# Kernel optimization log

Hardware: AMD Instinct MI355X
Metric: run time of the kernel (lower is better)

## Reference

```python
import jax, jax.numpy as jnp
import numpy as np

B, L, H, W = 4, 5000, 256, 256
C_IN, DIM_LOI, N_PTS0, N_PTS1, DIM_FC, N_OUT_LINE = 256, 128, 32, 8, 1024, 2500
SCALE = N_PTS0 // N_PTS1  # MaxPool1d kernel/stride


def setup_inputs() -> dict:
    key = jax.random.key(0)
    ks = jax.random.split(key, 8)
    feature = jax.random.normal(ks[0], (B, C_IN, H, W), jnp.float32)
    # line endpoints in pixel coords of the 256x256 feature map
    lines = jax.random.uniform(ks[1], (B, L, 2, 2), jnp.float32) * (H - 1)
    s = lambda fan: 1.0 / np.sqrt(fan)
    fc1_w = (jax.random.normal(ks[2], (DIM_LOI, C_IN), jnp.float32) * s(C_IN))
    fc1_b = jnp.zeros((DIM_LOI,), jnp.float32)
    w1 = jax.random.normal(ks[3], (DIM_LOI * N_PTS1, DIM_FC), jnp.float32) * s(DIM_LOI * N_PTS1)
    b1 = jnp.zeros((DIM_FC,), jnp.float32)
    w2 = jax.random.normal(ks[4], (DIM_FC, DIM_FC), jnp.float32) * s(DIM_FC)
    b2 = jnp.zeros((DIM_FC,), jnp.float32)
    w3 = jax.random.normal(ks[5], (DIM_FC, 4), jnp.float32) * s(DIM_FC)
    b3 = jnp.zeros((4,), jnp.float32)
    return dict(feature=feature, lines=lines, fc1_w=fc1_w, fc1_b=fc1_b,
                w1=w1, b1=b1, w2=w2, b2=b2, w3=w3, b3=b3)


def reference(feature, lines, fc1_w, fc1_b, w1, b1, w2, b2, w3, b3):
    # fc1: 1x1 conv  [B,C_IN,H,W] -> [B,DIM_LOI,H,W]
    x = jnp.einsum('bchw,oc->bohw', feature, fc1_w) + fc1_b[None, :, None, None]

    # sample N_PTS0 points along each line (lerp between endpoints), minus 0.5
    lam = jnp.linspace(0.0, 1.0, N_PTS0, dtype=feature.dtype)[None, None, :, None]
    p = lines[:, :, 0:1, :] * lam + lines[:, :, 1:2, :] * (1.0 - lam) - 0.5  # [B,L,P,2]
    px, py = p[..., 0], p[..., 1]  # px indexes H (rows), py indexes W (cols)
    px0 = jnp.clip(jnp.floor(px), 0.0, H - 1.0)
    py0 = jnp.clip(jnp.floor(py), 0.0, W - 1.0)
    px1 = jnp.clip(px0 + 1.0, 0.0, H - 1.0)
    py1 = jnp.clip(py0 + 1.0, 0.0, W - 1.0)
    ix0, iy0 = px0.astype(jnp.int32), py0.astype(jnp.int32)
    ix1, iy1 = px1.astype(jnp.int32), py1.astype(jnp.int32)
    idx00 = ix0 * W + iy0
    idx10 = ix1 * W + iy0
    idx01 = ix0 * W + iy1
    idx11 = ix1 * W + iy1
    w00 = (px1 - px) * (py1 - py)
    w10 = (px - px0) * (py1 - py)
    w01 = (px1 - px) * (py - py0)
    w11 = (px - px0) * (py - py0)

    def gather_one(fmap, i00, i10, i01, i11, g00, g10, g01, g11):
        f = fmap.reshape(DIM_LOI, H * W)
        g = lambda idx: f[:, idx.reshape(-1)].reshape(DIM_LOI, L, N_PTS0)
        return g(i00) * g00 + g(i10) * g10 + g(i01) * g01 + g(i11) * g11

    xp = jax.vmap(gather_one)(x, idx00, idx10, idx01, idx11, w00, w10, w01, w11)
    # xp: [B, DIM_LOI, L, N_PTS0] -> maxpool along points -> [B, DIM_LOI, L, N_PTS1]
    xp = xp.reshape(B, DIM_LOI, L, N_PTS1, SCALE).max(-1)
    # reshape like torch: [N, DIM_LOI, N_PTS1] -> [N, DIM_LOI*N_PTS1] (channel-major)
    feat = xp.transpose(0, 2, 1, 3).reshape(B, L, DIM_LOI * N_PTS1)

    # fc2 MLP -> 4 logits
    h = jax.nn.relu(feat @ w1 + b1)
    h = jax.nn.relu(h @ w2 + b2)
    logits = h @ w3 + b3  # [B, L, 4]
    s = jax.nn.softmax(logits, axis=-1)

    # threshold conditions
    keep = ((s[..., 1] > 0.25) | (s[..., 2] > 0.25) | (s[..., 3] > 0.25)) & (s[..., 0] < 0.25)

    def select(p0, s0, m):
        cnt = m.sum()
        key = jnp.where(m, jnp.argmax(s0, -1), -1)  # masked-out get -1 -> sorted last
        order = jnp.argsort(-key)  # stable desc sort of argmax class
        idx = order[jnp.arange(N_OUT_LINE) % jnp.maximum(cnt, 1)]
        lo = jnp.where(cnt > 0, p0[idx], 0.0)
        so = jnp.where(cnt > 0, s0[idx], 0.0)
        return lo, so

    lines_out, score_out = jax.vmap(select)(lines, s, keep)
    return lines_out, score_out, s
```

## Files before the change

### kernel.cpp

```cpp
#include <hip/hip_runtime.h>
#include <cstdint>
#include <cstddef>

#define B_     4
#define L_     5000
#define H_     256
#define W_     256
#define HW_    65536
#define CIN_   256
#define DLOI_  128
#define NPTS0_ 32
#define NPTS1_ 8
#define DFC_   1024
#define NOUT_  2500
#define M_     (B_*L_)
#define MPAD_  20096
#define NBAND_ 157

typedef _Float16 f16;
typedef _Float16 f16x4 __attribute__((ext_vector_type(4)));
typedef _Float16 f16x8 __attribute__((ext_vector_type(8)));
typedef float    f32x4 __attribute__((ext_vector_type(4)));

__device__ __forceinline__ void gload16(const void* g, void* l) {
  __builtin_amdgcn_global_load_lds(
      (const __attribute__((address_space(1))) void*)g,
      (__attribute__((address_space(3))) void*)l, 16, 0, 0);
}

__global__ __launch_bounds__(256) void k_wsplit(const float* __restrict__ src,
                                                f16* __restrict__ h,
                                                f16* __restrict__ l) {
  int i = (blockIdx.x * 256 + threadIdx.x) * 4;
  float4 v = *(const float4*)(src + i);
  f16 h0 = (f16)v.x, h1 = (f16)v.y, h2 = (f16)v.z, h3 = (f16)v.w;
  *(f16x4*)(h + i) = (f16x4){h0, h1, h2, h3};
  *(f16x4*)(l + i) = (f16x4){(f16)(v.x - (float)h0), (f16)(v.y - (float)h1),
                             (f16)(v.z - (float)h2), (f16)(v.w - (float)h3)};
}

__global__ __launch_bounds__(1024) void k_order(const float* __restrict__ lines,
                                                int* __restrict__ perm) {
  __shared__ int hist[64];
  __shared__ int off[64];
  const int b = blockIdx.x;
  const int t = threadIdx.x;
  if (t < 64) hist[t] = 0;
  __syncthreads();
  int mycell[5];
  #pragma unroll
  for (int i = 0; i < 5; i++) {
    const int l = t * 5 + i;
    int cell = -1;
    if (l < L_) {
      const float* ln = lines + (size_t)(b * L_ + l) * 4;
      float mx = 0.5f * (ln[0] + ln[2]);
      float my = 0.5f * (ln[1] + ln[3]);
      int cx = min(max((int)mx, 0), 255) >> 5;
      int cy = min(max((int)my, 0), 255) >> 5;
      cell = (cx & 1) | ((cy & 1) << 1) | ((cx & 2) << 1) | ((cy & 2) << 2)
           | ((cx & 4) << 2) | ((cy & 4) << 3);
      atomicAdd(&hist[cell], 1);
    }
    mycell[i] = cell;
  }
  __syncthreads();
  if (t == 0) {
    int s = 0;
    for (int c = 0; c < 64; c++) { off[c] = s; s += hist[c]; }
  }
  __syncthreads();
  #pragma unroll
  for (int i = 0; i < 5; i++) {
    if (mycell[i] >= 0) {
      int slot = atomicAdd(&off[mycell[i]], 1);
      perm[b * L_ + slot] = t * 5 + i;
    }
  }
}

__global__ __launch_bounds__(256) void k_conv_mfma(const float* __restrict__ fin,
                                                   const f16* __restrict__ wh,
                                                   const f16* __restrict__ wl,
                                                   const float* __restrict__ bias,
                                                   float* __restrict__ xout) {
  __shared__ f16 lds[16384];
  const int t = threadIdx.x;
  const int P0 = blockIdx.x * 128;
  const int b  = P0 >> 16;
  const int ph0 = P0 & 65535;
  const int lane = t & 63, wave = t >> 6;
  const int quad = lane >> 4, lo = lane & 15;
  const int wm = wave >> 1, wn = wave & 1;

  const int c_base = (t & 7) * 4;
  const int p = (t >> 3) * 4;
  const size_t fbase = (size_t)b * CIN_ * HW_ + (size_t)ph0 + p;

  const int srow = t >> 2;
  const int skb  = (t & 3) * 16;
  const char* gBh = (const char*)wh + (size_t)srow * 512 + skb;
  const char* gBl = (const char*)wl + (size_t)srow * 512 + skb;
  char* ldsB = (char*)lds + t * 16;

  f32x4 acc[4][4];
  #pragma unroll
  for (int mt = 0; mt < 4; mt++)
    #pragma unroll
    for (int nt = 0; nt < 4; nt++) acc[mt][nt] = (f32x4){0.f, 0.f, 0.f, 0.f};

  float4 av[4], nv[4];
  #pragma unroll
  for (int j = 0; j < 4; j++)
    av[j] = *(const float4*)(fin + fbase + (size_t)(c_base + j) * HW_);

  for (int kc = 0; kc < 8; kc++) {
    const size_t bko = (size_t)kc * 64;
    gload16(gBh + bko,         ldsB + 16384);
    gload16(gBh + 32768 + bko, ldsB + 16384 + 4096);
    gload16(gBl + bko,         ldsB + 24576);
    gload16(gBl + 32768 + bko, ldsB + 24576 + 4096);

    #pragma unroll
    for (int i = 0; i < 4; i++) {
      f16 hh[4], ll[4];
      #pragma unroll
      for (int j = 0; j < 4; j++) {
        float v = ((const float*)&av[j])[i];
        hh[j] = (f16)v;
        ll[j] = (f16)(v - (float)hh[j]);
      }
      *(f16x4*)(&lds[(p + i) * 32 + c_base])        = (f16x4){hh[0], hh[1], hh[2], hh[3]};
      *(f16x4*)(&lds[4096 + (p + i) * 32 + c_base]) = (f16x4){ll[0], ll[1], ll[2], ll[3]};
    }
    __syncthreads();

    if (kc < 7) {
      #pragma unroll
      for (int j = 0; j < 4; j++)
        nv[j] = *(const float4*)(fin + fbase + (size_t)((kc + 1) * 32 + c_base + j) * HW_);
    }

    f16x8 ah[4], al[4], bh4[4], bl4[4];
    #pragma unroll
    for (int mt = 0; mt < 4; mt++) {
      int row = wm * 64 + mt * 16 + lo;
      ah[mt] = *(const f16x8*)(&lds[row * 32 + quad * 8]);
      al[mt] = *(const f16x8*)(&lds[4096 + row * 32 + quad * 8]);
    }
    #pragma unroll
    for (int nt = 0; nt < 4; nt++) {
      int row = wn * 64 + nt * 16 + lo;
      bh4[nt] = *(const f16x8*)(&lds[8192 + row * 32 + quad * 8]);
      bl4[nt] = *(const f16x8*)(&lds[12288 + row * 32 + quad * 8]);
    }
    #pragma unroll
    for (int mt = 0; mt < 4; mt++)
      #pragma unroll
      for (int nt = 0; nt < 4; nt++) {
        acc[mt][nt] = __builtin_amdgcn_mfma_f32_16x16x32_f16(ah[mt], bh4[nt], acc[mt][nt], 0, 0, 0);
        acc[mt][nt] = __builtin_amdgcn_mfma_f32_16x16x32_f16(ah[mt], bl4[nt], acc[mt][nt], 0, 0, 0);
        acc[mt][nt] = __builtin_amdgcn_mfma_f32_16x16x32_f16(al[mt], bh4[nt], acc[mt][nt], 0, 0, 0);
      }
    __syncthreads();
    #pragma unroll
    for (int j = 0; j < 4; j++) av[j] = nv[j];
  }

  #pragma unroll
  for (int nt = 0; nt < 4; nt++) {
    int col = wn * 64 + nt * 16 + lo;
    float bv = bias[col];
    #pragma unroll
    for (int mt = 0; mt < 4; mt++) {
      int rowb = P0 + wm * 64 + mt * 16 + quad * 4;
      #pragma unroll
      for (int r = 0; r < 4; r++)
        xout[(size_t)(rowb + r) * DLOI_ + col] = acc[mt][nt][r] + bv;
    }
  }
}

__global__ __launch_bounds__(128) void k_sample(const float* __restrict__ x,
                                                const float* __restrict__ lines,
                                                const int* __restrict__ perm,
                                                f16* __restrict__ fh,
                                                f16* __restrict__ fl) {
  __shared__ int4   s_off[NPTS0_];
  __shared__ float4 s_wt [NPTS0_];
  const int blk0 = blockIdx.x;
  const int s = (blk0 & 7) * (M_ / 8) + (blk0 >> 3);
  const int b = s / L_;
  const int row = b * L_ + perm[s];
  const int c = threadIdx.x;
  const float* ln = lines + (size_t)row * 4;

  if (c < NPTS0_) {
    const float e0x = ln[0], e0y = ln[1], e1x = ln[2], e1y = ln[3];
    const int i = c;
    float lam = (float)i * (1.0f / 31.0f);
    float px = e0x * lam + e1x * (1.f - lam) - 0.5f;
    float py = e0y * lam + e1y * (1.f - lam) - 0.5f;
    float px0 = fminf(fmaxf(floorf(px), 0.f), 255.f);
    float py0 = fminf(fmaxf(floorf(py), 0.f), 255.f);
    float px1 = fminf(px0 + 1.f, 255.f);
    float py1 = fminf(py0 + 1.f, 255.f);
    int ix0 = (int)px0, iy0 = (int)py0, ix1 = (int)px1, iy1 = (int)py1;
    s_wt[i]  = make_float4((px1 - px) * (py1 - py),
                           (px - px0) * (py1 - py),
                           (px1 - px) * (py - py0),
                           (px - px0) * (py - py0));
    s_off[i] = make_int4((ix0 * W_ + iy0) * (DLOI_ * 4),
                         (ix1 * W_ + iy0) * (DLOI_ * 4),
                         (ix0 * W_ + iy1) * (DLOI_ * 4),
                         (ix1 * W_ + iy1) * (DLOI_ * 4));
  }
  __syncthreads();

  const char* xbc = (const char*)(x + (size_t)b * HW_ * DLOI_) + c * 4;
  f16x8 vh, vl;
  for (int q = 0; q < NPTS1_; q++) {
    float m = -1e30f;
    #pragma unroll
    for (int r = 0; r < 4; r++) {
      const int i = q * 4 + r;
      const int4   o = s_off[i];
      const float4 w = s_wt[i];
      float v = w.x * *(const float*)(xbc + o.x)
              + w.y * *(const float*)(xbc + o.y)
              + w.z * *(const float*)(xbc + o.z)
              + w.w * *(const float*)(xbc + o.w);
      m = fmaxf(m, v);
    }
    f16 h = (f16)m;
    vh[q] = h;
    vl[q] = (f16)(m - (float)h);
  }
  *(f16x8*)(fh + (size_t)row * DFC_ + c * 8) = vh;
  *(f16x8*)(fl + (size_t)row * DFC_ + c * 8) = vl;
}

__global__ __launch_bounds__(256) void k_tsplit(const float* __restrict__ Wsrc,
                                                f16* __restrict__ Th,
                                                f16* __restrict__ Tl) {
  __shared__ float tile[32][33];
  const int bj = blockIdx.x, bi = blockIdx.y;
  const int tx = threadIdx.x & 31, ty = threadIdx.x >> 5;
  #pragma unroll
  for (int r = ty; r < 32; r += 8)
    tile[r][tx] = Wsrc[(size_t)(bi * 32 + r) * 1024 + bj * 32 + tx];
  __syncthreads();
  #pragma unroll
  for (int r = ty; r < 32; r += 8) {
    float v = tile[tx][r];
    f16 h = (f16)v;
    size_t o = (size_t)(bj * 32 + r) * 1024 + bi * 32 + tx;
    Th[o] = h;
    Tl[o] = (f16)(v - (float)h);
  }
}

#define BKT_    32
#define NTT_    (DFC_/BKT_)
#define SLOT_B_ 32768
#define AH_O_   0
#define AL_O_   8192
#define BH_O_   16384
#define BL_O_   24576

template <bool SPLIT_OUT>
__global__ __launch_bounds__(256, 2) void k_gemm_f16x3(
    const f16* __restrict__ Ah, const f16* __restrict__ Al,
    const f16* __restrict__ Bh, const f16* __restrict__ Bl,
    const float* __restrict__ bias,
    f16* __restrict__ Oh, f16* __restrict__ Ol,
    const float* __restrict__ w3, float* __restrict__ part) {
  __shared__ f16 lds[2 * SLOT_B_ / 2];
  char* ldsc = (char*)lds;

  const int orig = blockIdx.x;
  const int wg = (orig & 7) * 157 + (orig >> 3);
  const int band = wg >> 3;
  const int nb   = wg & 7;
  const int r0 = band * 128;
  const int n0 = nb * 128;

  const int t = threadIdx.x;
  const int lane = t & 63, wave = t >> 6;
  const int quad = lane >> 4, lo = lane & 15;
  const int wm = wave >> 1, wn = wave & 1;

  const uint32_t u0 = (uint32_t)t;
  const uint32_t u1 = (uint32_t)t + 256u;
  const uint32_t us0 = u0 ^ ((u0 >> 3) & 7);
  const uint32_t us1 = u1 ^ ((u1 >> 3) & 7);
  const size_t s0 = (size_t)(us0 >> 2) * 2048 + (size_t)(us0 & 3) * 16;
  const size_t s1 = (size_t)(us1 >> 2) * 2048 + (size_t)(us1 & 3) * 16;

  const char* gAh = (const char*)Ah + (size_t)r0 * 2048;
  const char* gAl = (const char*)Al + (size_t)r0 * 2048;
  const char* gBh = (const char*)Bh + (size_t)n0 * 2048;
  const char* gBl = (const char*)Bl + (size_t)n0 * 2048;

  const int d0 = t * 16;
  const int d1 = 4096 + t * 16;

  int roffA[4], roffB[4];
  #pragma unroll
  for (int mt = 0; mt < 4; mt++) {
    int r = wm * 64 + mt * 16 + lo;
    roffA[mt] = (((r * 4 + quad) ^ ((r >> 1) & 7)) << 4);
  }
  #pragma unroll
  for (int nt = 0; nt < 4; nt++) {
    int r = wn * 64 + nt * 16 + lo;
    roffB[nt] = (((r * 4 + quad) ^ ((r >> 1) & 7)) << 4);
  }

  f32x4 acc[4][4];
  #pragma unroll
  for (int mt = 0; mt < 4; mt++)
    #pragma unroll
    for (int nt = 0; nt < 4; nt++) acc[mt][nt] = (f32x4){0.f, 0.f, 0.f, 0.f};

  gload16(gAh + s0, ldsc + AH_O_ + d0);
  gload16(gAh + s1, ldsc + AH_O_ + d1);
  gload16(gAl + s0, ldsc + AL_O_ + d0);
  gload16(gAl + s1, ldsc + AL_O_ + d1);
  gload16(gBh + s0, ldsc + BH_O_ + d0);
  gload16(gBh + s1, ldsc + BH_O_ + d1);
  gload16(gBl + s0, ldsc + BL_O_ + d0);
  gload16(gBl + s1, ldsc + BL_O_ + d1);
  asm volatile("s_waitcnt vmcnt(0)" ::: "memory");
  __builtin_amdgcn_s_barrier();

  for (int tt = 0; tt < NTT_; ++tt) {
    const char* sc = ldsc + (tt & 1) * SLOT_B_;
    char* sw = ldsc + ((tt + 1) & 1) * SLOT_B_;
    const size_t go = (size_t)(tt + 1) * 64;
    const bool pf = (tt + 1 < NTT_);

    if (pf) {
      gload16(gAh + go + s0, sw + AH_O_ + d0);
      gload16(gAh + go + s1, sw + AH_O_ + d1);
      gload16(gAl + go + s0, sw + AL_O_ + d0);
      gload16(gAl + go + s1, sw + AL_O_ + d1);
      gload16(gBh + go + s0, sw + BH_O_ + d0);
      gload16(gBh + go + s1, sw + BH_O_ + d1);
      gload16(gBl + go + s0, sw + BL_O_ + d0);
      gload16(gBl + go + s1, sw + BL_O_ + d1);
    }

    f16x8 ah[4], bh[4], al[4], bl[4];
    #pragma unroll
    for (int mt = 0; mt < 4; mt++)
      ah[mt] = *(const f16x8*)(sc + AH_O_ + roffA[mt]);
    #pragma unroll
    for (int nt = 0; nt < 4; nt++)
      bh[nt] = *(const f16x8*)(sc + BH_O_ + roffB[nt]);
    #pragma unroll
    for (int mt = 0; mt < 4; mt++)
      al[mt] = *(const f16x8*)(sc + AL_O_ + roffA[mt]);
    #pragma unroll
    for (int nt = 0; nt < 4; nt++)
      bl[nt] = *(const f16x8*)(sc + BL_O_ + roffB[nt]);

    __builtin_amdgcn_s_setprio(1);
    #pragma unroll
    for (int mt = 0; mt < 4; mt++)
      #pragma unroll
      for (int nt = 0; nt < 4; nt++)
        acc[mt][nt] = __builtin_amdgcn_mfma_f32_16x16x32_f16(ah[mt], bh[nt], acc[mt][nt], 0, 0, 0);
    #pragma unroll
    for (int mt = 0; mt < 4; mt++)
      #pragma unroll
      for (int nt = 0; nt < 4; nt++)
        acc[mt][nt] = __builtin_amdgcn_mfma_f32_16x16x32_f16(al[mt], bh[nt], acc[mt][nt], 0, 0, 0);
    #pragma unroll
    for (int mt = 0; mt < 4; mt++)
      #pragma unroll
      for (int nt = 0; nt < 4; nt++)
        acc[mt][nt] = __builtin_amdgcn_mfma_f32_16x16x32_f16(ah[mt], bl[nt], acc[mt][nt], 0, 0, 0);
    __builtin_amdgcn_s_setprio(0);

    if (pf) asm volatile("s_waitcnt vmcnt(0)" ::: "memory");
    __builtin_amdgcn_s_barrier();
  }

  if (SPLIT_OUT) {
    char* ep = ldsc + wave * 16384;
    #pragma unroll
    for (int mt = 0; mt < 4; mt++)
      #pragma unroll
      for (int nt = 0; nt < 4; nt++) {
        const int col = n0 + wn * 64 + nt * 16 + lo;
        const float bv = bias[col];
        const int col_l = nt * 16 + lo;
        #pragma unroll
        for (int r = 0; r < 4; r++) {
          const int rl = mt * 16 + quad * 4 + r;
          float v = fmaxf(acc[mt][nt][r] + bv, 0.f);
          f16 h = (f16)v;
          f16 lw = (f16)(v - (float)h);
          const int byte = rl * 128 + ((((col_l >> 3) ^ (rl & 7)) << 4)) + (col_l & 7) * 2;
          *(f16*)(ep + byte) = h;
          *(f16*)(ep + 8192 + byte) = lw;
        }
      }
    asm volatile("s_waitcnt lgkmcnt(0)" ::: "memory");
    __builtin_amdgcn_sched_barrier(0);
    const int r8 = lane >> 3;
    const int ck = lane & 7;
    #pragma unroll
    for (int g = 0; g < 8; g++) {
      const int rl = g * 8 + r8;
      const int grow = r0 + wm * 64 + rl;
      const int swz = ((ck ^ (rl & 7)) << 4);
      f16x8 vh = *(const f16x8*)(ep + rl * 128 + swz);
      f16x8 vl = *(const f16x8*)(ep + 8192 + rl * 128 + swz);
      if (grow < M_) {
        const size_t gb = (size_t)grow * 2048 + (size_t)(n0 + wn * 64) * 2 + ck * 16;
        *(f16x8*)((char*)Oh + gb) = vh;
        *(f16x8*)((char*)Ol + gb) = vl;
      }
    }
  } else {
    const int slot = nb * 2 + wn;
    #pragma unroll
    for (int mt = 0; mt < 4; mt++) {
      float p[4][4];
      #pragma unroll
      for (int r = 0; r < 4; r++)
        #pragma unroll
        for (int j = 0; j < 4; j++) p[r][j] = 0.f;
      #pragma unroll
      for (int nt = 0; nt < 4; nt++) {
        const int col = n0 + wn * 64 + nt * 16 + lo;
        const float bv = bias[col];
        float4 wv = *(const float4*)(w3 + col * 4);
        #pragma unroll
        for (int r = 0; r < 4; r++) {
          float v = fmaxf(acc[mt][nt][r] + bv, 0.f);
          p[r][0] = fmaf(v, wv.x, p[r][0]);
          p[r][1] = fmaf(v, wv.y, p[r][1]);
          p[r][2] = fmaf(v, wv.z, p[r][2]);
          p[r][3] = fmaf(v, wv.w, p[r][3]);
        }
      }
      #pragma unroll
      for (int r = 0; r < 4; r++)
        #pragma unroll
        for (int j = 0; j < 4; j++) {
          p[r][j] += __shfl_xor(p[r][j], 1);
          p[r][j] += __shfl_xor(p[r][j], 2);
          p[r][j] += __shfl_xor(p[r][j], 4);
          p[r][j] += __shfl_xor(p[r][j], 8);
        }
      if (lo == 0) {
        const int rowb = r0 + wm * 64 + mt * 16 + quad * 4;
        #pragma unroll
        for (int r = 0; r < 4; r++)
          *(float4*)(part + ((size_t)slot * MPAD_ + rowb + r) * 4) =
              make_float4(p[r][0], p[r][1], p[r][2], p[r][3]);
      }
    }
  }
}

__global__ __launch_bounds__(256) void k_head2(const float* __restrict__ part,
                                               const float* __restrict__ b3,
                                               float* __restrict__ s_out,
                                               int* __restrict__ key_out) {
  const int row = blockIdx.x * 256 + threadIdx.x;
  if (row >= M_) return;
  float l0 = b3[0], l1 = b3[1], l2 = b3[2], l3 = b3[3];
  #pragma unroll
  for (int sl = 0; sl < 16; sl++) {
    float4 p = *(const float4*)(part + ((size_t)sl * MPAD_ + row) * 4);
    l0 += p.x; l1 += p.y; l2 += p.z; l3 += p.w;
  }
  float mx = fmaxf(fmaxf(l0, l1), fmaxf(l2, l3));
  float e0 = expf(l0 - mx), e1 = expf(l1 - mx), e2 = expf(l2 - mx), e3 = expf(l3 - mx);
  float inv = 1.f / (e0 + e1 + e2 + e3);
  float s0 = e0 * inv, s1 = e1 * inv, s2 = e2 * inv, s3 = e3 * inv;
  *(float4*)(s_out + (size_t)row * 4) = make_float4(s0, s1, s2, s3);
  bool keep = ((s1 > 0.25f) || (s2 > 0.25f) || (s3 > 0.25f)) && (s0 < 0.25f);
  int am = 0; float best = s0;
  if (s1 > best) { best = s1; am = 1; }
  if (s2 > best) { best = s2; am = 2; }
  if (s3 > best) { best = s3; am = 3; }
  key_out[row] = keep ? am : -1;
}

__global__ __launch_bounds__(1024) void k_select(const int* __restrict__ key,
                                                 const float* __restrict__ lines,
                                                 const float* __restrict__ s,
                                                 float* __restrict__ out_lines,
                                                 float* __restrict__ out_score) {
  __shared__ int s_ord[L_];
  __shared__ int s_scan[1024];
  __shared__ int s_tot[5];
  const int b = blockIdx.x;
  const int t = threadIdx.x;
  const int base_l = t * 5;
  int cls[5];
  int c[5] = {0, 0, 0, 0, 0};
  #pragma unroll
  for (int i = 0; i < 5; i++) {
    int l = base_l + i;
    int cl = -1;
    if (l < L_) {
      int k = key[b * L_ + l];
      cl = (k < 0) ? 4 : (3 - k);
      c[cl]++;
    }
    cls[i] = cl;
  }
  int pf[5];
  for (int cc = 0; cc < 5; cc++) {
    s_scan[t] = c[cc];
    __syncthreads();
    for (int off = 1; off < 1024; off <<= 1) {
      int add = (t >= off) ? s_scan[t - off] : 0;
      __syncthreads();
      s_scan[t] += add;
      __syncthreads();
    }
    pf[cc] = s_scan[t] - c[cc];
    if (t == 1023) s_tot[cc] = s_scan[1023];
    __syncthreads();
  }
  int basec[5];
  basec[0] = 0;
  #pragma unroll
  for (int cc = 1; cc < 5; cc++) basec[cc] = basec[cc - 1] + s_tot[cc - 1];
  int run[5] = {0, 0, 0, 0, 0};
  #pragma unroll
  for (int i = 0; i < 5; i++) {
    if (cls[i] >= 0) {
      int cl = cls[i];
      int pos = basec[cl] + pf[cl] + run[cl];
      run[cl]++;
      s_ord[pos] = base_l + i;
    }
  }
  const int cnt = L_ - s_tot[4];
  __syncthreads();
  for (int j = t; j < NOUT_; j += 1024) {
    float4 lv = make_float4(0.f, 0.f, 0.f, 0.f);
    float4 sv = make_float4(0.f, 0.f, 0.f, 0.f);
    if (cnt > 0) {
      int idx = s_ord[j % cnt];
      lv = *(const float4*)(lines + (size_t)(b * L_ + idx) * 4);
      sv = *(const float4*)(s + (size_t)(b * L_ + idx) * 4);
    }
    *(float4*)(out_lines + (size_t)(b * NOUT_ + j) * 4) = lv;
    *(float4*)(out_score + (size_t)(b * NOUT_ + j) * 4) = sv;
  }
}

extern "C" void kernel_launch(void* const* d_in, const int* in_sizes, int n_in,
                              void* d_out, int out_size, void* d_ws, size_t ws_size,
                              hipStream_t stream) {
  const float* feature = (const float*)d_in[0];
  const float* lines   = (const float*)d_in[1];
  const float* fc1_w   = (const float*)d_in[2];
  const float* fc1_b   = (const float*)d_in[3];
  const float* w1      = (const float*)d_in[4];
  const float* b1      = (const float*)d_in[5];
  const float* w2      = (const float*)d_in[6];
  const float* b2      = (const float*)d_in[7];
  const float* w3      = (const float*)d_in[8];
  const float* b3      = (const float*)d_in[9];

  float* out_lines = (float*)d_out;
  float* out_score = out_lines + B_ * NOUT_ * 4;
  float* s_out     = out_score + B_ * NOUT_ * 4;

  char* ws = (char*)d_ws;
  float* x    = (float*)(ws);
  f16*   h1h  = (f16*)(ws);
  f16*   h1l  = (f16*)(ws + 41156608ull);
  float* part = (float*)(ws + 82313216ull);
  f16*   fh   = (f16*)(ws + 134217728ull);
  f16*   fl   = (f16*)(ws + 134217728ull + 41156608ull);
  f16*   wt1h = (f16*)(ws + 216530944ull);
  f16*   wt1l = (f16*)(ws + 216530944ull + 2097152ull);
  f16*   wt2h = (f16*)(ws + 216530944ull + 2ull * 2097152ull);
  f16*   wt2l = (f16*)(ws + 216530944ull + 3ull * 2097152ull);
  int*   keys = (int*)(ws + 224919552ull);
  f16*   wc_h = (f16*)(ws + 224999552ull);
  f16*   wc_l = (f16*)(ws + 224999552ull + 65536ull);

  k_order<<<dim3(B_), 1024, 0, stream>>>(lines, keys);
  k_wsplit<<<dim3(32), 256, 0, stream>>>(fc1_w, wc_h, wc_l);
  k_tsplit<<<dim3(32, 32), 256, 0, stream>>>(w1, wt1h, wt1l);
  k_tsplit<<<dim3(32, 32), 256, 0, stream>>>(w2, wt2h, wt2l);
  k_conv_mfma<<<dim3((B_ * HW_) / 128), 256, 0, stream>>>(feature, wc_h, wc_l, fc1_b, x);
  k_sample<<<dim3(M_), 128, 0, stream>>>(x, lines, keys, fh, fl);
  k_gemm_f16x3<true><<<dim3(1256), 256, 0, stream>>>(
      fh, fl, wt1h, wt1l, b1, h1h, h1l, nullptr, nullptr);
  k_gemm_f16x3<false><<<dim3(1256), 256, 0, stream>>>(
      h1h, h1l, wt2h, wt2l, b2, nullptr, nullptr, w3, part);
  k_head2<<<dim3((M_ + 255) / 256), 256, 0, stream>>>(part, b3, s_out, keys);
  k_select<<<dim3(B_), 1024, 0, stream>>>(keys, lines, s_out, out_lines, out_score);
}
```

Measured before the change: 827.1 us.

## Use two-wave 128x128 GEMM blocks with 128x64 per-wave tiles

Both f16x3 GEMM kernels now run with 128 threads (2 waves) per block instead of 256. Each wave owns a 128x64 output tile (8x4 MFMA subtiles) rather than 64x64, and each thread issues 4 global-to-LDS loads per operand instead of 2. The aim is more MFMA work per LDS read of B, which raises arithmetic intensity per wave. In exchange, accumulator registers double, launch bounds drop to 1 block per CU hint, and fewer waves are available to hide latency.

```diff
diff --git a/kernel.cpp b/kernel.cpp
--- a/kernel.cpp
+++ b/kernel.cpp
@@ -269,7 +269,7 @@
 #define BL_O_   24576
 
 template <bool SPLIT_OUT>
-__global__ __launch_bounds__(256, 2) void k_gemm_f16x3(
+__global__ __launch_bounds__(128, 1) void k_gemm_f16x3(
     const f16* __restrict__ Ah, const f16* __restrict__ Al,
     const f16* __restrict__ Bh, const f16* __restrict__ Bl,
     const float* __restrict__ bias,
@@ -288,49 +288,46 @@
   const int t = threadIdx.x;
   const int lane = t & 63, wave = t >> 6;
   const int quad = lane >> 4, lo = lane & 15;
-  const int wm = wave >> 1, wn = wave & 1;
-
-  const uint32_t u0 = (uint32_t)t;
-  const uint32_t u1 = (uint32_t)t + 256u;
-  const uint32_t us0 = u0 ^ ((u0 >> 3) & 7);
-  const uint32_t us1 = u1 ^ ((u1 >> 3) & 7);
-  const size_t s0 = (size_t)(us0 >> 2) * 2048 + (size_t)(us0 & 3) * 16;
-  const size_t s1 = (size_t)(us1 >> 2) * 2048 + (size_t)(us1 & 3) * 16;
+
+  size_t ssrc[4]; int sdst[4];
+  #pragma unroll
+  for (int pp = 0; pp < 4; pp++) {
+    const uint32_t u = (uint32_t)(pp * 128 + t);
+    const uint32_t us = u ^ ((u >> 3) & 7);
+    ssrc[pp] = (size_t)(us >> 2) * 2048 + (size_t)(us & 3) * 16;
+    sdst[pp] = pp * 2048 + t * 16;
+  }
 
   const char* gAh = (const char*)Ah + (size_t)r0 * 2048;
   const char* gAl = (const char*)Al + (size_t)r0 * 2048;
   const char* gBh = (const char*)Bh + (size_t)n0 * 2048;
   const char* gBl = (const char*)Bl + (size_t)n0 * 2048;
 
-  const int d0 = t * 16;
-  const int d1 = 4096 + t * 16;
-
-  int roffA[4], roffB[4];
-  #pragma unroll
-  for (int mt = 0; mt < 4; mt++) {
-    int r = wm * 64 + mt * 16 + lo;
+  int roffA[8], roffB[4];
+  #pragma unroll
+  for (int mt = 0; mt < 8; mt++) {
+    int r = mt * 16 + lo;
     roffA[mt] = (((r * 4 + quad) ^ ((r >> 1) & 7)) << 4);
   }
   #pragma unroll
   for (int nt = 0; nt < 4; nt++) {
-    int r = wn * 64 + nt * 16 + lo;
+    int r = wave * 64 + nt * 16 + lo;
     roffB[nt] = (((r * 4 + quad) ^ ((r >> 1) & 7)) << 4);
   }
 
-  f32x4 acc[4][4];
-  #pragma unroll
-  for (int mt = 0; mt < 4; mt++)
+  f32x4 acc[8][4];
+  #pragma unroll
+  for (int mt = 0; mt < 8; mt++)
     #pragma unroll
     for (int nt = 0; nt < 4; nt++) acc[mt][nt] = (f32x4){0.f, 0.f, 0.f, 0.f};
 
-  gload16(gAh + s0, ldsc + AH_O_ + d0);
-  gload16(gAh + s1, ldsc + AH_O_ + d1);
-  gload16(gAl + s0, ldsc + AL_O_ + d0);
-  gload16(gAl + s1, ldsc + AL_O_ + d1);
-  gload16(gBh + s0, ldsc + BH_O_ + d0);
-  gload16(gBh + s1, ldsc + BH_O_ + d1);
-  gload16(gBl + s0, ldsc + BL_O_ + d0);
-  gload16(gBl + s1, ldsc + BL_O_ + d1);
+  #pragma unroll
+  for (int pp = 0; pp < 4; pp++) {
+    gload16(gAh + ssrc[pp], ldsc + AH_O_ + sdst[pp]);
+    gload16(gAl + ssrc[pp], ldsc + AL_O_ + sdst[pp]);
+    gload16(gBh + ssrc[pp], ldsc + BH_O_ + sdst[pp]);
+    gload16(gBl + ssrc[pp], ldsc + BL_O_ + sdst[pp]);
+  }
   asm volatile("s_waitcnt vmcnt(0)" ::: "memory");
   __builtin_amdgcn_s_barrier();
 
@@ -341,46 +338,38 @@
     const bool pf = (tt + 1 < NTT_);
 
     if (pf) {
-      gload16(gAh + go + s0, sw + AH_O_ + d0);
-      gload16(gAh + go + s1, sw + AH_O_ + d1);
-      gload16(gAl + go + s0, sw + AL_O_ + d0);
-      gload16(gAl + go + s1, sw + AL_O_ + d1);
-      gload16(gBh + go + s0, sw + BH_O_ + d0);
-      gload16(gBh + go + s1, sw + BH_O_ + d1);
-      gload16(gBl + go + s0, sw + BL_O_ + d0);
-      gload16(gBl + go + s1, sw + BL_O_ + d1);
-    }
-
-    f16x8 ah[4], bh[4], al[4], bl[4];
-    #pragma unroll
-    for (int mt = 0; mt < 4; mt++)
-      ah[mt] = *(const f16x8*)(sc + AH_O_ + roffA[mt]);
+      #pragma unroll
+      for (int pp = 0; pp < 4; pp++) {
+        gload16(gAh + go + ssrc[pp], sw + AH_O_ + sdst[pp]);
+        gload16(gAl + go + ssrc[pp], sw + AL_O_ + sdst[pp]);
+        gload16(gBh + go + ssrc[pp], sw + BH_O_ + sdst[pp]);
+        gload16(gBl + go + ssrc[pp], sw + BL_O_ + sdst[pp]);
+      }
+    }
+
+    f16x8 bh[4], bl[4];
     #pragma unroll
     for (int nt = 0; nt < 4; nt++)
       bh[nt] = *(const f16x8*)(sc + BH_O_ + roffB[nt]);
     #pragma unroll
-    for (int mt = 0; mt < 4; mt++)
-      al[mt] = *(const f16x8*)(sc + AL_O_ + roffA[mt]);
-    #pragma unroll
     for (int nt = 0; nt < 4; nt++)
       bl[nt] = *(const f16x8*)(sc + BL_O_ + roffB[nt]);
 
     __builtin_amdgcn_s_setprio(1);
     #pragma unroll
-    for (int mt = 0; mt < 4; mt++)
+    for (int mt = 0; mt < 8; mt++) {
+      f16x8 ah = *(const f16x8*)(sc + AH_O_ + roffA[mt]);
+      f16x8 al = *(const f16x8*)(sc + AL_O_ + roffA[mt]);
       #pragma unroll
       for (int nt = 0; nt < 4; nt++)
-        acc[mt][nt] = __builtin_amdgcn_mfma_f32_16x16x32_f16(ah[mt], bh[nt], acc[mt][nt], 0, 0, 0);
-    #pragma unroll
-    for (int mt = 0; mt < 4; mt++)
+        acc[mt][nt] = __builtin_amdgcn_mfma_f32_16x16x32_f16(ah, bh[nt], acc[mt][nt], 0, 0, 0);
       #pragma unroll
       for (int nt = 0; nt < 4; nt++)
-        acc[mt][nt] = __builtin_amdgcn_mfma_f32_16x16x32_f16(al[mt], bh[nt], acc[mt][nt], 0, 0, 0);
-    #pragma unroll
-    for (int mt = 0; mt < 4; mt++)
+        acc[mt][nt] = __builtin_amdgcn_mfma_f32_16x16x32_f16(al, bh[nt], acc[mt][nt], 0, 0, 0);
       #pragma unroll
       for (int nt = 0; nt < 4; nt++)
-        acc[mt][nt] = __builtin_amdgcn_mfma_f32_16x16x32_f16(ah[mt], bl[nt], acc[mt][nt], 0, 0, 0);
+        acc[mt][nt] = __builtin_amdgcn_mfma_f32_16x16x32_f16(ah, bl[nt], acc[mt][nt], 0, 0, 0);
+    }
     __builtin_amdgcn_s_setprio(0);
 
     if (pf) asm volatile("s_waitcnt vmcnt(0)" ::: "memory");
@@ -388,12 +377,12 @@
   }
 
   if (SPLIT_OUT) {
-    char* ep = ldsc + wave * 16384;
-    #pragma unroll
-    for (int mt = 0; mt < 4; mt++)
+    char* ep = ldsc + wave * 32768;
+    #pragma unroll
+    for (int mt = 0; mt < 8; mt++)
       #pragma unroll
       for (int nt = 0; nt < 4; nt++) {
-        const int col = n0 + wn * 64 + nt * 16 + lo;
+        const int col = n0 + wave * 64 + nt * 16 + lo;
         const float bv = bias[col];
         const int col_l = nt * 16 + lo;
         #pragma unroll
@@ -404,7 +393,7 @@
           f16 lw = (f16)(v - (float)h);
           const int byte = rl * 128 + ((((col_l >> 3) ^ (rl & 7)) << 4)) + (col_l & 7) * 2;
           *(f16*)(ep + byte) = h;
-          *(f16*)(ep + 8192 + byte) = lw;
+          *(f16*)(ep + 16384 + byte) = lw;
         }
       }
     asm volatile("s_waitcnt lgkmcnt(0)" ::: "memory");
@@ -412,22 +401,22 @@
     const int r8 = lane >> 3;
     const int ck = lane & 7;
     #pragma unroll
-    for (int g = 0; g < 8; g++) {
+    for (int g = 0; g < 16; g++) {
       const int rl = g * 8 + r8;
-      const int grow = r0 + wm * 64 + rl;
+      const int grow = r0 + rl;
       const int swz = ((ck ^ (rl & 7)) << 4);
       f16x8 vh = *(const f16x8*)(ep + rl * 128 + swz);
-      f16x8 vl = *(const f16x8*)(ep + 8192 + rl * 128 + swz);
+      f16x8 vl = *(const f16x8*)(ep + 16384 + rl * 128 + swz);
       if (grow < M_) {
-        const size_t gb = (size_t)grow * 2048 + (size_t)(n0 + wn * 64) * 2 + ck * 16;
+        const size_t gb = (size_t)grow * 2048 + (size_t)(n0 + wave * 64) * 2 + ck * 16;
         *(f16x8*)((char*)Oh + gb) = vh;
         *(f16x8*)((char*)Ol + gb) = vl;
       }
     }
   } else {
-    const int slot = nb * 2 + wn;
-    #pragma unroll
-    for (int mt = 0; mt < 4; mt++) {
+    const int slot = nb * 2 + wave;
+    #pragma unroll
+    for (int mt = 0; mt < 8; mt++) {
       float p[4][4];
       #pragma unroll
       for (int r = 0; r < 4; r++)
@@ -435,7 +424,7 @@
         for (int j = 0; j < 4; j++) p[r][j] = 0.f;
       #pragma unroll
       for (int nt = 0; nt < 4; nt++) {
-        const int col = n0 + wn * 64 + nt * 16 + lo;
+        const int col = n0 + wave * 64 + nt * 16 + lo;
         const float bv = bias[col];
         float4 wv = *(const float4*)(w3 + col * 4);
         #pragma unroll
@@ -457,7 +446,7 @@
           p[r][j] += __shfl_xor(p[r][j], 8);
         }
       if (lo == 0) {
-        const int rowb = r0 + wm * 64 + mt * 16 + quad * 4;
+        const int rowb = r0 + mt * 16 + quad * 4;
         #pragma unroll
         for (int r = 0; r < 4; r++)
           *(float4*)(part + ((size_t)slot * MPAD_ + rowb + r) * 4) =
@@ -598,9 +587,9 @@
   k_tsplit<<<dim3(32, 32), 256, 0, stream>>>(w2, wt2h, wt2l);
   k_conv_mfma<<<dim3((B_ * HW_) / 128), 256, 0, stream>>>(feature, wc_h, wc_l, fc1_b, x);
   k_sample<<<dim3(M_), 128, 0, stream>>>(x, lines, keys, fh, fl);
-  k_gemm_f16x3<true><<<dim3(1256), 256, 0, stream>>>(
+  k_gemm_f16x3<true><<<dim3(1256), 128, 0, stream>>>(
       fh, fl, wt1h, wt1l, b1, h1h, h1l, nullptr, nullptr);
-  k_gemm_f16x3<false><<<dim3(1256), 256, 0, stream>>>(
+  k_gemm_f16x3<false><<<dim3(1256), 128, 0, stream>>>(
       h1h, h1l, wt2h, wt2l, b2, nullptr, nullptr, w3, part);
   k_head2<<<dim3((M_ + 255) / 256), 256, 0, stream>>>(part, b3, s_out, keys);
   k_select<<<dim3(B_), 1024, 0, stream>>>(keys, lines, s_out, out_lines, out_score);
```

New measurement: 895.8 us. +8.3%, slower.
